# Kernel tuning notes

Measured on AMD Instinct MI355X. Metric: run time of the kernel, lower is better.

## Reference

```python
import jax, jax.numpy as jnp
import numpy as np

N = 10000
D1, D2, D3, N_INPUT = 20, 256, 128, 500


def setup_inputs() -> dict:
    key = jax.random.key(0)
    k1, k2, k3, k4, k5 = jax.random.split(key, 5)
    z_igae = jax.random.normal(k1, (N, D1), dtype=jnp.float32)
    # row-stochastic-ish dense (normalized) adjacency stand-in
    adj = jax.random.uniform(k2, (N, N), dtype=jnp.float32) / N
    w3 = jax.random.normal(k3, (D1, D2), dtype=jnp.float32) * 0.1
    w4 = jax.random.normal(k4, (D2, D3), dtype=jnp.float32) * 0.1
    w5 = jax.random.normal(k5, (D3, N_INPUT), dtype=jnp.float32) * 0.1
    return {"z_igae": z_igae, "adj": adj, "w3": w3, "w4": w4, "w5": w5}


def reference(z_igae, adj, w3, w4, w5):
    # GNNLayer: spmm(adj, x @ W), tanh activation when active=True
    z = jnp.tanh(adj @ (z_igae @ w3))        # [N, D2]
    z = jnp.tanh(adj @ (z @ w4))             # [N, D3]
    z_hat = adj @ (z @ w5)                   # [N, n_input], active=False
    z_hat_adj = jax.nn.sigmoid(z_hat @ z_hat.T)  # [N, N] dense reconstruction
    return (z_hat, z_hat_adj)
```

## Files before the change

### kernel.cpp

```cpp
#include <hip/hip_runtime.h>
#include <cstddef>
#include <cstdint>


typedef __attribute__((ext_vector_type(8))) short bf16x8;
typedef __attribute__((ext_vector_type(4))) float f32x4;

__device__ inline unsigned short f2bf(float f) {
  union { float f; unsigned int u; } a; a.f = f;
  unsigned int u = a.u;
  u += 0x7fffu + ((u >> 16) & 1u);
  return (unsigned short)(u >> 16);
}

__device__ inline void gl_lds16(const void* g, void* l) {
  __builtin_amdgcn_global_load_lds(
      (const __attribute__((address_space(1))) void*)g,
      (__attribute__((address_space(3))) void*)l, 16, 0, 0);
}

template <int NT, int ACT>
__global__ __launch_bounds__(256)
void gemm_bf16(const short* __restrict__ A, int lda,
               const short* __restrict__ Bt, int ldb,
               float* __restrict__ C, long long cSplitStride, int ldc,
               int M, int Nvalid, int kChunks, int S) {
  __shared__ short As[64 * 64];
  __shared__ short Bs[NT * 64];
  const int tid  = threadIdx.x;
  const int wave = tid >> 6;
  const int lane = tid & 63;
  const int row0 = blockIdx.y * 64;
  const int col0 = blockIdx.x * NT;
  const int s    = blockIdx.z;
  const int t0 = (int)((long long)s * kChunks / S);
  const int t1 = (int)((long long)(s + 1) * kChunks / S);

  f32x4 acc[NT / 16];
#pragma unroll
  for (int i = 0; i < NT / 16; ++i) acc[i] = (f32x4){0.f, 0.f, 0.f, 0.f};

  const int lr = lane >> 3;
  const int lk = (((lane & 7) ^ lr)) * 8;

  const int fr = lane & 15;
  const int fq = lane >> 4;
  const int sw = lane & 7;

  for (int t = t0; t < t1; ++t) {
    const int k0 = t * 64;
    __syncthreads();
#pragma unroll
    for (int i = 0; i < 2; ++i) {
      int c = wave + 4 * i;
      gl_lds16(A + (size_t)(row0 + 8 * c + lr) * lda + k0 + lk,
               (void*)(As + c * 512));
    }
#pragma unroll
    for (int i = 0; i < NT / 32; ++i) {
      int c = wave + 4 * i;
      gl_lds16(Bt + (size_t)(col0 + 8 * c + lr) * ldb + k0 + lk,
               (void*)(Bs + c * 512));
    }
    __syncthreads();
#pragma unroll
    for (int ks = 0; ks < 2; ++ks) {
      const int go = ((ks * 4 + fq) ^ sw) * 8;
      bf16x8 af = *(const bf16x8*)&As[(wave * 16 + fr) * 64 + go];
#pragma unroll
      for (int nt = 0; nt < NT / 16; ++nt) {
        bf16x8 bfr = *(const bf16x8*)&Bs[(nt * 16 + fr) * 64 + go];
        acc[nt] = __builtin_amdgcn_mfma_f32_16x16x32_bf16(af, bfr, acc[nt], 0, 0, 0);
      }
    }
  }

  float* Cs = C + (long long)s * cSplitStride;
  const int rbase = row0 + wave * 16 + (lane >> 4) * 4;
  const int cbase = col0 + (lane & 15);
#pragma unroll
  for (int nt = 0; nt < NT / 16; ++nt) {
    const int cc = cbase + nt * 16;
#pragma unroll
    for (int r = 0; r < 4; ++r) {
      const int rr = rbase + r;
      float v = acc[nt][r];
      if (ACT == 2) {
        v = 1.0f / (1.0f + __expf(-v));
        if (rr < M && cc < Nvalid) Cs[(size_t)rr * ldc + cc] = v;
      } else {
        Cs[(size_t)rr * ldc + cc] = v;
      }
    }
  }
}

#define TK 16
#define TM 64
#define TN 64

template <int ACT, bool OBF16>
__global__ __launch_bounds__(256)
void gemm_nn_f32(const float* __restrict__ A, int lda,
                 const float* __restrict__ B, int ldb,
                 void* __restrict__ Cp, int ldc, int M, int N, int K) {
  __shared__ float Asm[TK][TM + 4];
  __shared__ float Bsm[TK][TN + 4];
  const int tid = threadIdx.x;
  const int tx = tid & 15, ty = tid >> 4;
  const int row0 = blockIdx.y * TM, col0 = blockIdx.x * TN;
  const int a_m = tid >> 2, a_k = (tid & 3) << 2;
  const int b_k = tid >> 4, b_n = (tid & 15) << 2;
  float acc[4][4] = {};
  const int ntile = (K + TK - 1) / TK;

  auto ld_a = [&](int k0) {
    float4 v = make_float4(0.f, 0.f, 0.f, 0.f);
    int r = row0 + a_m, k = k0 + a_k;
    if (r < M && k + 3 < K + (K & 3 ? 0 : 0) && k + 3 < K)
      v = *(const float4*)(A + (size_t)r * lda + k);
    else if (r < M && k < K)
      v = *(const float4*)(A + (size_t)r * lda + k);
    return v;
  };
  auto ld_b = [&](int k0) {
    float4 v = make_float4(0.f, 0.f, 0.f, 0.f);
    int k = k0 + b_k, c = col0 + b_n;
    if (k < K && c + 3 < N) v = *(const float4*)(B + (size_t)k * ldb + c);
    return v;
  };

  float4 pa = ld_a(0), pb = ld_b(0);
  for (int t = 0; t < ntile; ++t) {
    __syncthreads();
    Asm[a_k + 0][a_m] = pa.x; Asm[a_k + 1][a_m] = pa.y;
    Asm[a_k + 2][a_m] = pa.z; Asm[a_k + 3][a_m] = pa.w;
    *(float4*)&Bsm[b_k][b_n] = pb;
    __syncthreads();
    if (t + 1 < ntile) { pa = ld_a((t + 1) * TK); pb = ld_b((t + 1) * TK); }
#pragma unroll
    for (int kk = 0; kk < TK; ++kk) {
      float4 a = *(const float4*)&Asm[kk][ty << 2];
      float4 b = *(const float4*)&Bsm[kk][tx << 2];
      float av[4] = {a.x, a.y, a.z, a.w};
      float bv[4] = {b.x, b.y, b.z, b.w};
#pragma unroll
      for (int i = 0; i < 4; ++i)
#pragma unroll
        for (int j = 0; j < 4; ++j) acc[i][j] += av[i] * bv[j];
    }
  }
#pragma unroll
  for (int i = 0; i < 4; ++i) {
    int r = row0 + (ty << 2) + i;
    if (r >= M) continue;
#pragma unroll
    for (int j = 0; j < 4; ++j) {
      int c = col0 + (tx << 2) + j;
      if (c >= N) continue;
      float v = acc[i][j];
      if (ACT == 1) v = tanhf(v);
      if (OBF16) ((unsigned short*)Cp)[(size_t)r * ldc + c] = f2bf(v);
      else       ((float*)Cp)[(size_t)r * ldc + c] = v;
    }
  }
}

template <int ACT>
__global__ __launch_bounds__(256)
void gemm_nt_f32(const float* __restrict__ A, int lda,
                 const float* __restrict__ B, int ldb,
                 float* __restrict__ C, int ldc, int M, int N, int K) {
  __shared__ float Asm[TK][TM + 4];
  __shared__ float Bsm[TK][TN + 4];
  const int tid = threadIdx.x;
  const int tx = tid & 15, ty = tid >> 4;
  const int row0 = blockIdx.y * TM, col0 = blockIdx.x * TN;
  const int a_m = tid >> 2, a_k = (tid & 3) << 2;
  const int b_n = tid >> 2, b_k = (tid & 3) << 2;
  float acc[4][4] = {};
  const int ntile = (K + TK - 1) / TK;

  auto ld_a = [&](int k0) {
    float4 v = make_float4(0.f, 0.f, 0.f, 0.f);
    int r = row0 + a_m, k = k0 + a_k;
    if (r < M && k + 3 < K) v = *(const float4*)(A + (size_t)r * lda + k);
    return v;
  };
  auto ld_b = [&](int k0) {
    float4 v = make_float4(0.f, 0.f, 0.f, 0.f);
    int c = col0 + b_n, k = k0 + b_k;
    if (c < N && k + 3 < K) v = *(const float4*)(B + (size_t)c * ldb + k);
    return v;
  };

  float4 pa = ld_a(0), pb = ld_b(0);
  for (int t = 0; t < ntile; ++t) {
    __syncthreads();
    Asm[a_k + 0][a_m] = pa.x; Asm[a_k + 1][a_m] = pa.y;
    Asm[a_k + 2][a_m] = pa.z; Asm[a_k + 3][a_m] = pa.w;
    Bsm[b_k + 0][b_n] = pb.x; Bsm[b_k + 1][b_n] = pb.y;
    Bsm[b_k + 2][b_n] = pb.z; Bsm[b_k + 3][b_n] = pb.w;
    __syncthreads();
    if (t + 1 < ntile) { pa = ld_a((t + 1) * TK); pb = ld_b((t + 1) * TK); }
#pragma unroll
    for (int kk = 0; kk < TK; ++kk) {
      float4 a = *(const float4*)&Asm[kk][ty << 2];
      float4 b = *(const float4*)&Bsm[kk][tx << 2];
      float av[4] = {a.x, a.y, a.z, a.w};
      float bv[4] = {b.x, b.y, b.z, b.w};
#pragma unroll
      for (int i = 0; i < 4; ++i)
#pragma unroll
        for (int j = 0; j < 4; ++j) acc[i][j] += av[i] * bv[j];
    }
  }
#pragma unroll
  for (int i = 0; i < 4; ++i) {
    int r = row0 + (ty << 2) + i;
    if (r >= M) continue;
#pragma unroll
    for (int j = 0; j < 4; ++j) {
      int c = col0 + (tx << 2) + j;
      if (c >= N) continue;
      C[(size_t)r * ldc + c] = acc[i][j];
    }
  }
}

#define NROWS 10000
#define MP 10048

__global__ void convert_adj(const float* __restrict__ adj, short* __restrict__ out) {
  int row = blockIdx.y;
  int c4 = (blockIdx.x * 256 + threadIdx.x) * 4;
  if (c4 >= MP) return;
  ushort4 o = {0, 0, 0, 0};
  if (row < NROWS && c4 < NROWS) {
    float4 v = *(const float4*)(adj + (size_t)row * NROWS + c4);
    o.x = f2bf(v.x); o.y = f2bf(v.y); o.z = f2bf(v.z); o.w = f2bf(v.w);
  }
  *(ushort4*)(out + (size_t)row * MP + c4) = o;
}

__global__ void tr_zigae(const float* __restrict__ z, short* __restrict__ zt) {
  int m = blockIdx.x * 256 + threadIdx.x;
  int n = blockIdx.y;
  if (m >= MP) return;
  float v = (n < 20 && m < NROWS) ? z[(size_t)m * 20 + n] : 0.f;
  zt[(size_t)n * MP + m] = f2bf(v);
}

__global__ void transpose_c128(const float* __restrict__ in, int M,
                               short* __restrict__ out) {
  __shared__ float tile[32][33];
  int m0 = blockIdx.x * 32, n0 = blockIdx.y * 32;
  int tx = threadIdx.x, ty = threadIdx.y;
  for (int i = ty; i < 32; i += 8) {
    int m = m0 + i;
    tile[i][tx] = (m < M) ? in[(size_t)m * 128 + n0 + tx] : 0.f;
  }
  __syncthreads();
  for (int i = ty; i < 32; i += 8) {
    int n = n0 + i, m = m0 + tx;
    if (m < MP) out[(size_t)n * MP + m] = f2bf(tile[tx][i]);
  }
}

__global__ void reduce_g1(const float* __restrict__ P, float* __restrict__ g1) {
  int m = blockIdx.x * 4 + (threadIdx.x >> 5);
  int n = threadIdx.x & 31;
  if (m >= NROWS) return;
  float s = 0.f;
#pragma unroll
  for (int i = 0; i < 8; ++i) s += P[(size_t)i * MP * 32 + (size_t)m * 32 + n];
  g1[(size_t)m * 32 + n] = s;
}

template <int ACT>
__global__ void reduce128(const float* __restrict__ P, float* __restrict__ outf,
                          short* __restrict__ outb, int M) {
  int m = blockIdx.x, n = threadIdx.x;
  if (m >= M) { if (outb) outb[(size_t)m * 128 + n] = 0; return; }
  float s = 0.f;
#pragma unroll
  for (int i = 0; i < 8; ++i) s += P[(size_t)i * MP * 128 + (size_t)m * 128 + n];
  if (ACT == 1) s = tanhf(s);
  if (outf) outf[(size_t)m * 128 + n] = s;
  if (outb) outb[(size_t)m * 128 + n] = f2bf(s);
}

__global__ void zero_bf16(short* p, int n) {
  int i = blockIdx.x * 256 + threadIdx.x;
  if (i < n) p[i] = 0;
}

extern "C" void kernel_launch(void* const* d_in, const int* in_sizes, int n_in,
                              void* d_out, int out_size, void* d_ws, size_t ws_size,
                              hipStream_t stream) {
  const float* z_igae = (const float*)d_in[0];
  const float* adj    = (const float*)d_in[1];
  const float* w3     = (const float*)d_in[2];
  const float* w4     = (const float*)d_in[3];
  const float* w5     = (const float*)d_in[4];

  const int M = NROWS, D2 = 256, D3 = 128, NI = 500;
  const int S = 8, KC = MP / 64;

  float* z_hat   = (float*)d_out;
  float* out_adj = (float*)d_out + (size_t)M * NI;

  char* oa = (char*)out_adj;
  short* adjb = (short*)oa;
  float* P    = (float*)(oa + 204ll * 1024 * 1024);
  char*  sc   = oa + 248ll * 1024 * 1024;
  float* z1   = (float*)(sc);
  float* t2   = (float*)(sc + 11ll * 1024 * 1024);
  short* t2t  = (short*)(sc + 17ll * 1024 * 1024);
  float* z2   = (float*)(sc + 20ll * 1024 * 1024);
  short* z2t  = (short*)(sc + 26ll * 1024 * 1024);
  float* g1   = (float*)(sc + 29ll * 1024 * 1024);
  short* zt   = (short*)(sc + 31ll * 1024 * 1024);
  float* Mm   = (float*)(sc + 32ll * 1024 * 1024);
  float* g3   = (float*)(sc + 33ll * 1024 * 1024);

  short* hb  = (short*)d_ws;
  short* g3b = (short*)d_ws + (size_t)MP * 128;

  dim3 blk(256);
  const int MT = 157;

  convert_adj<<<dim3(10, MP), blk, 0, stream>>>(adj, adjb);
  tr_zigae<<<dim3(40, 32), blk, 0, stream>>>(z_igae, zt);
  gemm_bf16<32, 0><<<dim3(1, MT, S), blk, 0, stream>>>(
      adjb, MP, zt, MP, P, (long long)MP * 32, 32, M, 32, KC, S);
  reduce_g1<<<dim3(2500), dim3(128), 0, stream>>>(P, g1);
  gemm_nn_f32<1, false><<<dim3(4, MT), blk, 0, stream>>>(g1, 32, w3, D2, z1, D2, M, D2, 20);
  gemm_nn_f32<0, false><<<dim3(2, MT), blk, 0, stream>>>(z1, D2, w4, D3, t2, D3, M, D3, D2);
  transpose_c128<<<dim3(314, 4), dim3(32, 8), 0, stream>>>(t2, M, t2t);
  gemm_bf16<128, 0><<<dim3(1, MT, S), blk, 0, stream>>>(
      adjb, MP, t2t, MP, P, (long long)MP * 128, 128, M, 128, KC, S);
  reduce128<1><<<dim3(M), dim3(128), 0, stream>>>(P, z2, (short*)nullptr, M);
  transpose_c128<<<dim3(314, 4), dim3(32, 8), 0, stream>>>(z2, M, z2t);
  gemm_bf16<128, 0><<<dim3(1, MT, S), blk, 0, stream>>>(
      adjb, MP, z2t, MP, P, (long long)MP * 128, 128, M, 128, KC, S);
  reduce128<0><<<dim3(10112), dim3(128), 0, stream>>>(P, g3, g3b, M);
  gemm_nn_f32<0, false><<<dim3(8, MT), blk, 0, stream>>>(g3, D3, w5, NI, z_hat, NI, M, NI, D3);
  gemm_nt_f32<0><<<dim3(2, 2), blk, 0, stream>>>(w5, NI, w5, NI, Mm, D3, D3, D3, NI);
  gemm_nn_f32<0, true><<<dim3(2, MT), blk, 0, stream>>>(g3, D3, Mm, D3, (void*)hb, D3, M, D3, D3);
  zero_bf16<<<dim3(24), blk, 0, stream>>>(hb + (size_t)M * 128, 48 * 128);
  gemm_bf16<128, 2><<<dim3(79, MT, 1), blk, 0, stream>>>(
      hb, 128, g3b, 128, out_adj, 0, M, M, M, 2, 1);
}
```

Before: 998.1 us.

## Fuse adj bf16 conversion into first GEMM, double-buffer LDS, larger recon tiles

```diff
diff --git a/kernel.cpp b/kernel.cpp
--- a/kernel.cpp
+++ b/kernel.cpp
@@ -5,6 +5,10 @@
 
 typedef __attribute__((ext_vector_type(8))) short bf16x8;
 typedef __attribute__((ext_vector_type(4))) float f32x4;
+
+#define NROWS 10000
+#define MP 10048
+#define MP2 10112
 
 __device__ inline unsigned short f2bf(float f) {
   union { float f; unsigned int u; } a; a.f = f;
@@ -19,14 +23,87 @@
       (__attribute__((address_space(3))) void*)l, 16, 0, 0);
 }
 
-template <int NT, int ACT>
+__global__ __launch_bounds__(256)
+void gemm1_fused(const float* __restrict__ adj, const short* __restrict__ zt,
+                 short* __restrict__ adjb, float* __restrict__ P,
+                 int kChunks, int S) {
+  __shared__ short As[64 * 64];
+  __shared__ short Bs[32 * 64];
+  const int tid  = threadIdx.x;
+  const int wave = tid >> 6;
+  const int lane = tid & 63;
+  const int row0 = blockIdx.y * 64;
+  const int s    = blockIdx.z;
+  const int t0 = (int)((long long)s * kChunks / S);
+  const int t1 = (int)((long long)(s + 1) * kChunks / S);
+
+  f32x4 acc[2];
+#pragma unroll
+  for (int i = 0; i < 2; ++i) acc[i] = (f32x4){0.f, 0.f, 0.f, 0.f};
+
+  const int lr = lane >> 3;
+  const int lk = ((lane & 7) ^ lr) * 8;
+  const int fr = lane & 15, fq = lane >> 4, sw = lane & 7;
+
+  const int ar  = tid >> 2;
+  const int acq = tid & 3;
+  const int gr  = row0 + ar;
+  const bool rv = gr < NROWS;
+
+  for (int t = t0; t < t1; ++t) {
+    const int k0 = t * 64;
+    __syncthreads();
+    gl_lds16(zt + (size_t)(8 * wave + lr) * MP + k0 + lk, (void*)(Bs + wave * 512));
+    const int gc = k0 + acq * 16;
+    float4 f[4];
+#pragma unroll
+    for (int j = 0; j < 4; ++j) {
+      int c = gc + 4 * j;
+      f[j] = (rv && c < NROWS) ? *(const float4*)(adj + (size_t)gr * NROWS + c)
+                               : make_float4(0.f, 0.f, 0.f, 0.f);
+    }
+    unsigned short h[16] __attribute__((aligned(16)));
+#pragma unroll
+    for (int j = 0; j < 4; ++j) {
+      h[4 * j + 0] = f2bf(f[j].x); h[4 * j + 1] = f2bf(f[j].y);
+      h[4 * j + 2] = f2bf(f[j].z); h[4 * j + 3] = f2bf(f[j].w);
+    }
+    *(uint4*)(adjb + (size_t)gr * MP + gc)     = *(const uint4*)&h[0];
+    *(uint4*)(adjb + (size_t)gr * MP + gc + 8) = *(const uint4*)&h[8];
+    *(bf16x8*)&As[ar * 64 + ((acq * 2 + 0) ^ (ar & 7)) * 8] = *(const bf16x8*)&h[0];
+    *(bf16x8*)&As[ar * 64 + ((acq * 2 + 1) ^ (ar & 7)) * 8] = *(const bf16x8*)&h[8];
+    __syncthreads();
+#pragma unroll
+    for (int ks = 0; ks < 2; ++ks) {
+      const int go = ((ks * 4 + fq) ^ sw) * 8;
+      bf16x8 af = *(const bf16x8*)&As[(wave * 16 + fr) * 64 + go];
+#pragma unroll
+      for (int nt = 0; nt < 2; ++nt) {
+        bf16x8 bfr = *(const bf16x8*)&Bs[(nt * 16 + fr) * 64 + go];
+        acc[nt] = __builtin_amdgcn_mfma_f32_16x16x32_bf16(af, bfr, acc[nt], 0, 0, 0);
+      }
+    }
+  }
+  float* Cs = P + (size_t)s * MP * 32;
+  const int rbase = row0 + wave * 16 + (lane >> 4) * 4;
+  const int cbase = lane & 15;
+#pragma unroll
+  for (int nt = 0; nt < 2; ++nt) {
+    const int cc = cbase + nt * 16;
+#pragma unroll
+    for (int r = 0; r < 4; ++r)
+      Cs[(size_t)(rbase + r) * 32 + cc] = acc[nt][r];
+  }
+}
+
+template <int NT>
 __global__ __launch_bounds__(256)
 void gemm_bf16(const short* __restrict__ A, int lda,
                const short* __restrict__ Bt, int ldb,
                float* __restrict__ C, long long cSplitStride, int ldc,
-               int M, int Nvalid, int kChunks, int S) {
-  __shared__ short As[64 * 64];
-  __shared__ short Bs[NT * 64];
+               int kChunks, int S) {
+  __shared__ short As[2][64 * 64];
+  __shared__ short Bs[2][NT * 64];
   const int tid  = threadIdx.x;
   const int wave = tid >> 6;
   const int lane = tid & 63;
@@ -41,35 +118,37 @@
   for (int i = 0; i < NT / 16; ++i) acc[i] = (f32x4){0.f, 0.f, 0.f, 0.f};
 
   const int lr = lane >> 3;
-  const int lk = (((lane & 7) ^ lr)) * 8;
-
-  const int fr = lane & 15;
-  const int fq = lane >> 4;
-  const int sw = lane & 7;
-
-  for (int t = t0; t < t1; ++t) {
+  const int lk = ((lane & 7) ^ lr) * 8;
+  const int fr = lane & 15, fq = lane >> 4, sw = lane & 7;
+
+  auto stage = [&](int b, int t) {
     const int k0 = t * 64;
-    __syncthreads();
 #pragma unroll
     for (int i = 0; i < 2; ++i) {
       int c = wave + 4 * i;
       gl_lds16(A + (size_t)(row0 + 8 * c + lr) * lda + k0 + lk,
-               (void*)(As + c * 512));
+               (void*)(&As[b][c * 512]));
     }
 #pragma unroll
     for (int i = 0; i < NT / 32; ++i) {
       int c = wave + 4 * i;
       gl_lds16(Bt + (size_t)(col0 + 8 * c + lr) * ldb + k0 + lk,
-               (void*)(Bs + c * 512));
-    }
-    __syncthreads();
+               (void*)(&Bs[b][c * 512]));
+    }
+  };
+
+  stage(0, t0);
+  for (int t = t0; t < t1; ++t) {
+    const int b = (t - t0) & 1;
+    __syncthreads();
+    if (t + 1 < t1) stage(b ^ 1, t + 1);
 #pragma unroll
     for (int ks = 0; ks < 2; ++ks) {
       const int go = ((ks * 4 + fq) ^ sw) * 8;
-      bf16x8 af = *(const bf16x8*)&As[(wave * 16 + fr) * 64 + go];
+      bf16x8 af = *(const bf16x8*)&As[b][(wave * 16 + fr) * 64 + go];
 #pragma unroll
       for (int nt = 0; nt < NT / 16; ++nt) {
-        bf16x8 bfr = *(const bf16x8*)&Bs[(nt * 16 + fr) * 64 + go];
+        bf16x8 bfr = *(const bf16x8*)&Bs[b][(nt * 16 + fr) * 64 + go];
         acc[nt] = __builtin_amdgcn_mfma_f32_16x16x32_bf16(af, bfr, acc[nt], 0, 0, 0);
       }
     }
@@ -82,14 +161,72 @@
   for (int nt = 0; nt < NT / 16; ++nt) {
     const int cc = cbase + nt * 16;
 #pragma unroll
-    for (int r = 0; r < 4; ++r) {
-      const int rr = rbase + r;
-      float v = acc[nt][r];
-      if (ACT == 2) {
-        v = 1.0f / (1.0f + __expf(-v));
-        if (rr < M && cc < Nvalid) Cs[(size_t)rr * ldc + cc] = v;
-      } else {
-        Cs[(size_t)rr * ldc + cc] = v;
+    for (int r = 0; r < 4; ++r)
+      Cs[(size_t)(rbase + r) * ldc + cc] = acc[nt][r];
+  }
+}
+
+__global__ __launch_bounds__(256)
+void gemm_recon(const short* __restrict__ A, const short* __restrict__ Bt,
+                float* __restrict__ C) {
+  __shared__ short As[128 * 64];
+  __shared__ short Bs[128 * 64];
+  const int tid  = threadIdx.x;
+  const int wave = tid >> 6;
+  const int lane = tid & 63;
+  const int row0 = blockIdx.y * 128;
+  const int col0 = blockIdx.x * 128;
+
+  f32x4 acc[2][8];
+#pragma unroll
+  for (int i = 0; i < 2; ++i)
+#pragma unroll
+    for (int j = 0; j < 8; ++j) acc[i][j] = (f32x4){0.f, 0.f, 0.f, 0.f};
+
+  const int lr = lane >> 3;
+  const int lk = ((lane & 7) ^ lr) * 8;
+  const int fr = lane & 15, fq = lane >> 4, sw = lane & 7;
+
+  for (int t = 0; t < 2; ++t) {
+    const int k0 = t * 64;
+    __syncthreads();
+#pragma unroll
+    for (int i = 0; i < 4; ++i) {
+      int c = wave + 4 * i;
+      gl_lds16(A + (size_t)(row0 + 8 * c + lr) * 128 + k0 + lk, (void*)(As + c * 512));
+      gl_lds16(Bt + (size_t)(col0 + 8 * c + lr) * 128 + k0 + lk, (void*)(Bs + c * 512));
+    }
+    __syncthreads();
+#pragma unroll
+    for (int ks = 0; ks < 2; ++ks) {
+      const int go = ((ks * 4 + fq) ^ sw) * 8;
+      bf16x8 a0 = *(const bf16x8*)&As[(wave * 32 + fr) * 64 + go];
+      bf16x8 a1 = *(const bf16x8*)&As[(wave * 32 + 16 + fr) * 64 + go];
+#pragma unroll
+      for (int nt = 0; nt < 8; ++nt) {
+        bf16x8 bfr = *(const bf16x8*)&Bs[(nt * 16 + fr) * 64 + go];
+        acc[0][nt] = __builtin_amdgcn_mfma_f32_16x16x32_bf16(a0, bfr, acc[0][nt], 0, 0, 0);
+        acc[1][nt] = __builtin_amdgcn_mfma_f32_16x16x32_bf16(a1, bfr, acc[1][nt], 0, 0, 0);
+      }
+    }
+  }
+
+  const int q = lane >> 4;
+#pragma unroll
+  for (int mf = 0; mf < 2; ++mf) {
+    const int rb = row0 + wave * 32 + mf * 16 + q * 4;
+#pragma unroll
+    for (int nt = 0; nt < 8; ++nt) {
+      const int cc = col0 + nt * 16 + (lane & 15);
+      if (cc >= NROWS) continue;
+#pragma unroll
+      for (int r = 0; r < 4; ++r) {
+        const int rr = rb + r;
+        if (rr < NROWS) {
+          float v = acc[mf][nt][r];
+          v = 1.0f / (1.0f + __expf(-v));
+          C[(size_t)rr * NROWS + cc] = v;
+        }
       }
     }
   }
@@ -117,10 +254,7 @@
   auto ld_a = [&](int k0) {
     float4 v = make_float4(0.f, 0.f, 0.f, 0.f);
     int r = row0 + a_m, k = k0 + a_k;
-    if (r < M && k + 3 < K + (K & 3 ? 0 : 0) && k + 3 < K)
-      v = *(const float4*)(A + (size_t)r * lda + k);
-    else if (r < M && k < K)
-      v = *(const float4*)(A + (size_t)r * lda + k);
+    if (r < M && k < K) v = *(const float4*)(A + (size_t)r * lda + k);
     return v;
   };
   auto ld_b = [&](int k0) {
@@ -228,20 +362,6 @@
   }
 }
 
-#define NROWS 10000
-#define MP 10048
-
-__global__ void convert_adj(const float* __restrict__ adj, short* __restrict__ out) {
-  int row = blockIdx.y;
-  int c4 = (blockIdx.x * 256 + threadIdx.x) * 4;
-  if (c4 >= MP) return;
-  ushort4 o = {0, 0, 0, 0};
-  if (row < NROWS && c4 < NROWS) {
-    float4 v = *(const float4*)(adj + (size_t)row * NROWS + c4);
-    o.x = f2bf(v.x); o.y = f2bf(v.y); o.z = f2bf(v.z); o.w = f2bf(v.w);
-  }
-  *(ushort4*)(out + (size_t)row * MP + c4) = o;
-}
 
 __global__ void tr_zigae(const float* __restrict__ z, short* __restrict__ zt) {
   int m = blockIdx.x * 256 + threadIdx.x;
@@ -277,6 +397,40 @@
   g1[(size_t)m * 32 + n] = s;
 }
 
+__global__ __launch_bounds__(256)
+void reduce_tr(const float* __restrict__ P, short* __restrict__ z2t) {
+  __shared__ float T[128][33];
+  const int tid = threadIdx.x;
+  const int m0 = blockIdx.x * 32;
+  const int mr = tid >> 5;
+  const int n0 = (tid & 31) * 4;
+#pragma unroll
+  for (int g = 0; g < 4; ++g) {
+    const int mm = g * 8 + mr;
+    const int m = m0 + mm;
+    f32x4 sAcc = (f32x4){0.f, 0.f, 0.f, 0.f};
+#pragma unroll
+    for (int i = 0; i < 8; ++i) {
+      f32x4 v = *(const f32x4*)(P + (size_t)i * MP * 128 + (size_t)m * 128 + n0);
+      sAcc += v;
+    }
+    if (m < NROWS) {
+      T[n0 + 0][mm] = tanhf(sAcc[0]); T[n0 + 1][mm] = tanhf(sAcc[1]);
+      T[n0 + 2][mm] = tanhf(sAcc[2]); T[n0 + 3][mm] = tanhf(sAcc[3]);
+    } else {
+      T[n0 + 0][mm] = 0.f; T[n0 + 1][mm] = 0.f;
+      T[n0 + 2][mm] = 0.f; T[n0 + 3][mm] = 0.f;
+    }
+  }
+  __syncthreads();
+  const int n = tid >> 1, mh = (tid & 1) * 16;
+  unsigned short h[16] __attribute__((aligned(16)));
+#pragma unroll
+  for (int j = 0; j < 16; ++j) h[j] = f2bf(T[n][mh + j]);
+  *(uint4*)(z2t + (size_t)n * MP + m0 + mh)     = *(const uint4*)&h[0];
+  *(uint4*)(z2t + (size_t)n * MP + m0 + mh + 8) = *(const uint4*)&h[8];
+}
+
 template <int ACT>
 __global__ void reduce128(const float* __restrict__ P, float* __restrict__ outf,
                           short* __restrict__ outb, int M) {
@@ -317,38 +471,33 @@
   float* z1   = (float*)(sc);
   float* t2   = (float*)(sc + 11ll * 1024 * 1024);
   short* t2t  = (short*)(sc + 17ll * 1024 * 1024);
-  float* z2   = (float*)(sc + 20ll * 1024 * 1024);
-  short* z2t  = (short*)(sc + 26ll * 1024 * 1024);
-  float* g1   = (float*)(sc + 29ll * 1024 * 1024);
-  short* zt   = (short*)(sc + 31ll * 1024 * 1024);
-  float* Mm   = (float*)(sc + 32ll * 1024 * 1024);
-  float* g3   = (float*)(sc + 33ll * 1024 * 1024);
+  short* z2t  = (short*)(sc + 20ll * 1024 * 1024);
+  float* g1   = (float*)(sc + 23ll * 1024 * 1024);
+  short* zt   = (short*)(sc + 25ll * 1024 * 1024);
+  float* Mm   = (float*)(sc + 26ll * 1024 * 1024);
+  float* g3   = (float*)(sc + 27ll * 1024 * 1024);
 
   short* hb  = (short*)d_ws;
-  short* g3b = (short*)d_ws + (size_t)MP * 128;
+  short* g3b = (short*)d_ws + (size_t)MP2 * 128;
 
   dim3 blk(256);
   const int MT = 157;
 
-  convert_adj<<<dim3(10, MP), blk, 0, stream>>>(adj, adjb);
   tr_zigae<<<dim3(40, 32), blk, 0, stream>>>(z_igae, zt);
-  gemm_bf16<32, 0><<<dim3(1, MT, S), blk, 0, stream>>>(
-      adjb, MP, zt, MP, P, (long long)MP * 32, 32, M, 32, KC, S);
+  gemm1_fused<<<dim3(1, MT, S), blk, 0, stream>>>(adj, zt, adjb, P, KC, S);
   reduce_g1<<<dim3(2500), dim3(128), 0, stream>>>(P, g1);
   gemm_nn_f32<1, false><<<dim3(4, MT), blk, 0, stream>>>(g1, 32, w3, D2, z1, D2, M, D2, 20);
   gemm_nn_f32<0, false><<<dim3(2, MT), blk, 0, stream>>>(z1, D2, w4, D3, t2, D3, M, D3, D2);
   transpose_c128<<<dim3(314, 4), dim3(32, 8), 0, stream>>>(t2, M, t2t);
-  gemm_bf16<128, 0><<<dim3(1, MT, S), blk, 0, stream>>>(
-      adjb, MP, t2t, MP, P, (long long)MP * 128, 128, M, 128, KC, S);
-  reduce128<1><<<dim3(M), dim3(128), 0, stream>>>(P, z2, (short*)nullptr, M);
-  transpose_c128<<<dim3(314, 4), dim3(32, 8), 0, stream>>>(z2, M, z2t);
-  gemm_bf16<128, 0><<<dim3(1, MT, S), blk, 0, stream>>>(
-      adjb, MP, z2t, MP, P, (long long)MP * 128, 128, M, 128, KC, S);
-  reduce128<0><<<dim3(10112), dim3(128), 0, stream>>>(P, g3, g3b, M);
+  gemm_bf16<128><<<dim3(1, MT, S), blk, 0, stream>>>(
+      adjb, MP, t2t, MP, P, (long long)MP * 128, 128, KC, S);
+  reduce_tr<<<dim3(314), blk, 0, stream>>>(P, z2t);
+  gemm_bf16<128><<<dim3(1, MT, S), blk, 0, stream>>>(
+      adjb, MP, z2t, MP, P, (long long)MP * 128, 128, KC, S);
+  reduce128<0><<<dim3(MP2), dim3(128), 0, stream>>>(P, g3, g3b, M);
   gemm_nn_f32<0, false><<<dim3(8, MT), blk, 0, stream>>>(g3, D3, w5, NI, z_hat, NI, M, NI, D3);
   gemm_nt_f32<0><<<dim3(2, 2), blk, 0, stream>>>(w5, NI, w5, NI, Mm, D3, D3, D3, NI);
   gemm_nn_f32<0, true><<<dim3(2, MT), blk, 0, stream>>>(g3, D3, Mm, D3, (void*)hb, D3, M, D3, D3);
-  zero_bf16<<<dim3(24), blk, 0, stream>>>(hb + (size_t)M * 128, 48 * 128);
-  gemm_bf16<128, 2><<<dim3(79, MT, 1), blk, 0, stream>>>(
-      hb, 128, g3b, 128, out_adj, 0, M, M, M, 2, 1);
-}
+  zero_bf16<<<dim3(56), blk, 0, stream>>>(hb + (size_t)M * 128, (MP2 - M) * 128);
+  gemm_recon<<<dim3(79, 79), blk, 0, stream>>>(hb, g3b, out_adj);
+}
```

Measured after the change: 1.023 ms. 1.03x slower.
